# Optimization experiments

Measured on AMD Instinct MI355X. Metric: run time of the kernel, lower is better.

The kernel has to match this reference:

```python
import jax, jax.numpy as jnp
import numpy as np

GROUPS = 8
EPS = 1e-5
STRIDE_W = 2


def group_norm(x, gamma, beta, groups=GROUPS):
    B, C, H, W = x.shape
    xr = x.reshape(B, groups, C // groups, H, W)
    m = xr.mean(axis=(2, 3, 4), keepdims=True)
    v = xr.var(axis=(2, 3, 4), keepdims=True)
    xn = ((xr - m) * jax.lax.rsqrt(v + EPS)).reshape(B, C, H, W)
    return xn * gamma[None, :, None, None] + beta[None, :, None, None]


def setup_inputs() -> dict:
    key = jax.random.key(0)
    ks = jax.random.split(key, 8)
    B, Cin, Cout = 2, 128, 256
    Hin, Win = 181, 360
    Hout, Wout = 91, 180
    K, NNZ = 7, 16  # piecewise-linear (3,3) basis -> 7 basis fns; 16 nonzeros per output row
    x = jax.random.normal(ks[0], (B, Cin, Hin, Win), jnp.float32)
    psi_vals = jax.random.normal(ks[1], (K, Hout, NNZ), jnp.float32) * 0.1
    psi_hi = jax.random.randint(ks[2], (Hout, NNZ), 0, Hin)
    psi_wi = jax.random.randint(ks[3], (Hout, NNZ), 0, Win)
    weight = jax.random.normal(ks[4], (Cout, Cin, K), jnp.float32) * (1.0 / np.sqrt(Cin * K))
    bias = jnp.zeros((Cout,), jnp.float32)
    gn1_gamma = jnp.ones((Cin,), jnp.float32)
    gn1_beta = jnp.zeros((Cin,), jnp.float32)
    w1 = jax.random.normal(ks[5], (2 * Cin, Cin), jnp.float32) * (1.0 / np.sqrt(Cin))
    b1 = jnp.zeros((2 * Cin,), jnp.float32)
    w2 = jax.random.normal(ks[6], (Cin, 2 * Cin), jnp.float32) * (1.0 / np.sqrt(2 * Cin))
    b2 = jnp.zeros((Cin,), jnp.float32)
    gamma2 = jnp.ones((Cout,), jnp.float32)
    beta2 = jnp.zeros((Cout,), jnp.float32)
    return dict(x=x, psi_vals=psi_vals, psi_hi=psi_hi, psi_wi=psi_wi, weight=weight,
                bias=bias, gn1_gamma=gn1_gamma, gn1_beta=gn1_beta, w1=w1, b1=b1,
                w2=w2, b2=b2, gamma2=gamma2, beta2=beta2)


def reference(x, psi_vals, psi_hi, psi_wi, weight, bias, gn1_gamma, gn1_beta,
              w1, b1, w2, b2, gamma2, beta2):
    B, C, Hin, Win = x.shape
    K, Hout, NNZ = psi_vals.shape
    Wout = Win // STRIDE_W

    # --- FlowerBlock stand-in (norm -> 1x1 expand -> GELU -> 1x1 project) + residual ---
    h = group_norm(x, gn1_gamma, gn1_beta)
    h = jnp.einsum('oc,bchw->bohw', w1, h) + b1[None, :, None, None]
    h = jax.nn.gelu(h)
    h = jnp.einsum('oc,bchw->bohw', w2, h) + b2[None, :, None, None]
    x = h + x
    skip = x

    # --- DISCO S2 conv: sparse basis-weighted gather + channel contraction ---
    # psi is longitudinally translation-equivariant: nonzeros stored for lon 0,
    wo = jnp.arange(Wout)
    idx = psi_hi[:, None, :] * Win + (psi_wi[:, None, :] + STRIDE_W * wo[None, :, None]) % Win  # [Hout,Wout,NNZ]
    xg = x.reshape(B, C, Hin * Win)[:, :, idx]               # [B,C,Hout,Wout,NNZ] gather
    y = jnp.einsum('khn,bchwn->bckhw', psi_vals, xg)          # basis-weighted reduce
    out = jnp.einsum('ock,bckhw->bohw', weight, y) + bias[None, :, None, None]

    x_down = jax.nn.gelu(group_norm(out, gamma2, beta2))
    return (skip, x_down)
```

## Files before the change

### kernel.cpp

```cpp
#include <hip/hip_runtime.h>


#define HW      65160
#define HIN     181
#define WIN     360
#define HOUT    91
#define WOUT    180
#define CIN     128
#define COUT    256
#define KB      7
#define NNZ     16
#define N_GN1   1042560
#define N_GN2   524160
#define NPB     16380

typedef float  f32x4  __attribute__((ext_vector_type(4)));
typedef __bf16 bf16x8 __attribute__((ext_vector_type(8)));

__device__ __forceinline__ unsigned short f2b(float v){
    return __builtin_bit_cast(unsigned short, (__bf16)v);
}
__device__ __forceinline__ unsigned pkbf(float a, float b){
    return (unsigned)__builtin_bit_cast(unsigned short, (__bf16)a)
         | ((unsigned)__builtin_bit_cast(unsigned short, (__bf16)b) << 16);
}
__device__ __forceinline__ float blo(unsigned u){ return __uint_as_float(u << 16); }
__device__ __forceinline__ float bhi(unsigned u){ return __uint_as_float(u & 0xffff0000u); }

__device__ __forceinline__ float gelu_f(float v){
    float z = v * __builtin_fmaf(0.0356774081363f, v*v, 0.7978845608028654f);
    float e = __builtin_amdgcn_exp2f(-2.8853900817779268f * z);
    return v * __builtin_amdgcn_rcpf(1.0f + e);
}

__global__ __launch_bounds__(256) void k_prep(
    const float* __restrict__ x, float* __restrict__ part,
    const float* __restrict__ wsrc, unsigned short* __restrict__ wbf,
    const float* __restrict__ w2, unsigned short* __restrict__ w2b)
{
    const int blk_id = blockIdx.x;
    const int t = threadIdx.x;

    if (blk_id < 2048){
        const int bg = blk_id >> 7, blk = blk_id & 127;
        const float4* p4 = (const float4*)(x + (size_t)bg * N_GN1);
        float s = 0.f, ss = 0.f;
        for (int v = blk*256 + t; v < N_GN1/4; v += 128*256){
            float4 q = p4[v];
            s  += q.x + q.y + q.z + q.w;
            ss += q.x*q.x + q.y*q.y + q.z*q.z + q.w*q.w;
        }
        #pragma unroll
        for (int off = 32; off; off >>= 1){ s += __shfl_down(s, off); ss += __shfl_down(ss, off); }
        __shared__ float ls[4][2];
        if ((t & 63) == 0){ ls[t>>6][0] = s; ls[t>>6][1] = ss; }
        __syncthreads();
        if (t == 0){
            s  = ls[0][0] + ls[1][0] + ls[2][0] + ls[3][0];
            ss = ls[0][1] + ls[1][1] + ls[2][1] + ls[3][1];
            part[(bg*128 + blk)*2]     = s;
            part[(bg*128 + blk)*2 + 1] = ss;
        }
    } else if (blk_id < 2304){
        const int co = blk_id - 2048;
        for (int r = t; r < 896; r += 256){
            int k = r >> 7, c = r & 127;
            wbf[co*896 + r] = f2b(wsrc[co*896 + c*7 + k]);
        }
    } else {
        const int i = (blk_id - 2304)*256 + t;
        if (i < 32768) w2b[i] = f2b(w2[i]);
    }
}

__global__ __launch_bounds__(64) void k_fold(
    const float* __restrict__ part,
    const float* __restrict__ w1, const float* __restrict__ b1,
    const float* __restrict__ g1, const float* __restrict__ be1,
    unsigned short* __restrict__ w1f, float* __restrict__ b1f)
{
    const int id = blockIdx.x;
    const int b = id >> 8, oc = id & 255;
    const int l = threadIdx.x;

    float mArr[8], rArr[8];
    #pragma unroll
    for (int g = 0; g < 8; ++g){
        const int bg = b*8 + g;
        float s  = part[(bg*128 + l)*2]     + part[(bg*128 + 64 + l)*2];
        float ss = part[(bg*128 + l)*2 + 1] + part[(bg*128 + 64 + l)*2 + 1];
        #pragma unroll
        for (int off = 32; off; off >>= 1){ s += __shfl_down(s, off); ss += __shfl_down(ss, off); }
        s = __shfl(s, 0); ss = __shfl(ss, 0);
        float m = s / (float)N_GN1;
        float v = ss / (float)N_GN1 - m*m;
        mArr[g] = m;
        rArr[g] = 1.0f / sqrtf(v + 1e-5f);
    }

    float acc = 0.f;
    #pragma unroll
    for (int j = 0; j < 2; ++j){
        const int c = l + j*64;
        const int g = c >> 4;
        float a  = rArr[g] * g1[c];
        float bb = be1[c] - mArr[g]*a;
        float wv = w1[oc*128 + c];
        w1f[((size_t)b*256 + oc)*128 + c] = f2b(wv * a);
        acc += wv * bb;
    }
    #pragma unroll
    for (int off = 32; off; off >>= 1) acc += __shfl_down(acc, off);
    if (l == 0) b1f[b*256 + oc] = b1[oc] + acc;
}

__global__ __launch_bounds__(256, 4) void k_mlp(
    const float* __restrict__ x,
    const unsigned short* __restrict__ w1f, const float* __restrict__ b1f,
    const unsigned short* __restrict__ w2b, const float* __restrict__ b2,
    float* __restrict__ skip, unsigned short* __restrict__ sbf)
{
    __shared__ unsigned short xns[64*128];
    __shared__ unsigned short h1h[64*128];

    const int t = threadIdx.x;
    const int b = blockIdx.y;
    const int pix0 = blockIdx.x * 64;
    const int valid = min(64, HW - pix0);

    const int w  = t >> 6, l = t & 63;
    const int lr = l & 15, lk = l >> 4;

    {
        const int p = l;
        const unsigned sw = ((unsigned)(p & 7)) << 4;
        const float* xb = x + (size_t)b*128*HW + pix0 + p;
        #pragma unroll
        for (int i = 0; i < 8; ++i){
            const int c0 = w*32 + i*4;
            uint2 pk;
            if (p < valid){
                pk.x = pkbf(xb[(size_t)(c0+0)*HW], xb[(size_t)(c0+1)*HW]);
                pk.y = pkbf(xb[(size_t)(c0+2)*HW], xb[(size_t)(c0+3)*HW]);
            } else { pk.x = 0u; pk.y = 0u; }
            *(uint2*)((char*)xns + p*256 + (((unsigned)(c0*2)) ^ sw)) = pk;
        }
    }
    __syncthreads();

    f32x4 acc2[4][2];
    {
        const float bv0 = b2[w*32 + lr];
        const float bv1 = b2[w*32 + 16 + lr];
        #pragma unroll
        for (int pm = 0; pm < 4; ++pm){
            acc2[pm][0] = (f32x4)bv0;
            acc2[pm][1] = (f32x4)bv1;
        }
    }

    const unsigned short* w1p = w1f + (size_t)b*256*128;

    #pragma unroll
    for (int half = 0; half < 2; ++half){
        {
            f32x4 acc1[2][4];
            #pragma unroll
            for (int m = 0; m < 2; ++m){
                float4 bv = *(const float4*)(b1f + b*256 + half*128 + w*32 + m*16 + lk*4);
                #pragma unroll
                for (int nf = 0; nf < 4; ++nf) acc1[m][nf] = __builtin_bit_cast(f32x4, bv);
            }
            const unsigned short* wr = w1p + (size_t)(half*128 + w*32 + lr)*128 + lk*8;
            #pragma unroll
            for (int ks = 0; ks < 4; ++ks){
                bf16x8 af[2];
                #pragma unroll
                for (int m = 0; m < 2; ++m)
                    af[m] = __builtin_bit_cast(bf16x8, *(const uint4*)(wr + m*16*128 + ks*32));
                bf16x8 bfv[4];
                #pragma unroll
                for (int nf = 0; nf < 4; ++nf){
                    const int p = nf*16 + lr;
                    unsigned off = (unsigned)(p*256)
                                 + (((unsigned)(ks*64 + lk*16)) ^ (((unsigned)(p & 7)) << 4));
                    bfv[nf] = __builtin_bit_cast(bf16x8, *(const uint4*)((const char*)xns + off));
                }
                #pragma unroll
                for (int m = 0; m < 2; ++m)
                    #pragma unroll
                    for (int nf = 0; nf < 4; ++nf)
                        acc1[m][nf] = __builtin_amdgcn_mfma_f32_16x16x32_bf16(af[m], bfv[nf], acc1[m][nf], 0, 0, 0);
            }
            #pragma unroll
            for (int m = 0; m < 2; ++m){
                const int oc0 = w*32 + m*16 + lk*4;
                #pragma unroll
                for (int nf = 0; nf < 4; ++nf){
                    const int p = nf*16 + lr;
                    uint2 pk;
                    pk.x = pkbf(gelu_f(acc1[m][nf][0]), gelu_f(acc1[m][nf][1]));
                    pk.y = pkbf(gelu_f(acc1[m][nf][2]), gelu_f(acc1[m][nf][3]));
                    unsigned off = (unsigned)(p*256)
                                 + (((unsigned)(oc0*2)) ^ (((unsigned)(p & 7)) << 4));
                    *(uint2*)((char*)h1h + off) = pk;
                }
            }
        }
        __syncthreads();

        {
            const unsigned short* wr = w2b + (size_t)(w*32 + lr)*256 + half*128 + lk*8;
            #pragma unroll
            for (int ks = 0; ks < 4; ++ks){
                bf16x8 bfw[2];
                #pragma unroll
                for (int cn = 0; cn < 2; ++cn)
                    bfw[cn] = __builtin_bit_cast(bf16x8, *(const uint4*)(wr + cn*16*256 + ks*32));
                bf16x8 afh[4];
                #pragma unroll
                for (int pm = 0; pm < 4; ++pm){
                    const int p = pm*16 + lr;
                    unsigned off = (unsigned)(p*256)
                                 + (((unsigned)(ks*64 + lk*16)) ^ (((unsigned)(p & 7)) << 4));
                    afh[pm] = __builtin_bit_cast(bf16x8, *(const uint4*)((const char*)h1h + off));
                }
                #pragma unroll
                for (int pm = 0; pm < 4; ++pm)
                    #pragma unroll
                    for (int cn = 0; cn < 2; ++cn)
                        acc2[pm][cn] = __builtin_amdgcn_mfma_f32_16x16x32_bf16(afh[pm], bfw[cn], acc2[pm][cn], 0, 0, 0);
            }
        }
        if (half == 0) __syncthreads();
    }

    #pragma unroll
    for (int pm = 0; pm < 4; ++pm){
        const int p0 = pm*16 + lk*4;
        if (p0 < valid){
            #pragma unroll
            for (int cn = 0; cn < 2; ++cn){
                const int c = w*32 + cn*16 + lr;
                size_t base = (size_t)(b*128 + c)*HW + pix0 + p0;
                float4 o;
                #pragma unroll
                for (int r = 0; r < 4; ++r){
                    const int p = p0 + r;
                    unsigned off = (unsigned)(p*256)
                                 + (((unsigned)(c*2)) ^ (((unsigned)(p & 7)) << 4));
                    unsigned short us = *(const unsigned short*)((const char*)xns + off);
                    ((float*)&o)[r] = acc2[pm][cn][r] + blo((unsigned)us);
                }
                *(float4*)(skip + base) = o;
                if (sbf){
                    unsigned short* sp = sbf + ((size_t)b*HW + pix0 + p0)*128 + c;
                    sp[0]   = f2b(o.x);
                    sp[128] = f2b(o.y);
                    sp[256] = f2b(o.z);
                    sp[384] = f2b(o.w);
                }
            }
        }
    }
}

__global__ __launch_bounds__(256) void k_dfuse(
    const unsigned short* __restrict__ sbf,
    const float* __restrict__ psi_v, const int* __restrict__ psi_hi, const int* __restrict__ psi_wi,
    const unsigned short* __restrict__ wbf, const float* __restrict__ bias,
    unsigned short* __restrict__ xdb, float* __restrict__ part)
{
    __shared__ unsigned short yT[64*256];
    __shared__ float psis[2][112];
    __shared__ int   his[2][16], wis[2][16];

    const int flat = blockIdx.x + 256*blockIdx.y;
    const int rem  = (flat & 7)*64 + (flat >> 3);
    const int nt   = rem & 255;
    const int b    = rem >> 8;
    const int n0   = nt*64;

    const int t = threadIdx.x;
    const int w = t >> 6, l = t & 63;
    const int lr = l & 15, lk = l >> 4;

    const int ho0 = n0 / WOUT;
    const int ho1 = min((n0 + 63) / WOUT, HOUT - 1);

    if (t < 112)        psis[0][t]       = psi_v[((t >> 4)*HOUT + ho0)*NNZ + (t & 15)];
    else if (t < 224)   psis[1][t - 112] = psi_v[(((t - 112) >> 4)*HOUT + ho1)*NNZ + ((t - 112) & 15)];
    else if (t < 240){  his[0][t - 224] = psi_hi[ho0*NNZ + t - 224];
                        wis[0][t - 224] = psi_wi[ho0*NNZ + t - 224]; }
    else             {  his[1][t - 240] = psi_hi[ho1*NNZ + t - 240];
                        wis[1][t - 240] = psi_wi[ho1*NNZ + t - 240]; }
    __syncthreads();

    const int row = t >> 2, cq = t & 3;
    const int n_c = min(n0 + row, NPB - 1);
    const int ho  = n_c / WOUT;
    const int wo  = n_c - ho*WOUT;
    const int sel = (ho == ho0) ? 0 : 1;
    const unsigned swr = ((unsigned)(row & 7)) << 4;

    int offs[16];
    #pragma unroll
    for (int n = 0; n < 16; ++n){
        int wv = wis[sel][n] + 2*wo;
        wv = (wv >= WIN) ? (wv - WIN) : wv;
        offs[n] = his[sel][n]*WIN + wv;
    }
    const unsigned short* sb = sbf + (size_t)b * HW * 128;

    f32x4 acc[4][4];
    #pragma unroll
    for (int i = 0; i < 4; ++i)
        #pragma unroll
        for (int j = 0; j < 4; ++j) acc[i][j] = (f32x4)0.f;

    #pragma unroll 1
    for (int cc = 0; cc < 4; ++cc){
        __syncthreads();
        {
            const int cl0 = cq*8;
            float ya[8][7];
            #pragma unroll
            for (int ci = 0; ci < 8; ++ci)
                #pragma unroll
                for (int k = 0; k < 7; ++k) ya[ci][k] = 0.f;

            #pragma unroll 4
            for (int n = 0; n < 16; ++n){
                uint4 q = *(const uint4*)(sb + (size_t)offs[n]*128 + cc*32 + cl0);
                float g0 = blo(q.x), g1 = bhi(q.x), g2 = blo(q.y), g3 = bhi(q.y);
                float g4 = blo(q.z), g5 = bhi(q.z), g6 = blo(q.w), g7 = bhi(q.w);
                #pragma unroll
                for (int k = 0; k < 7; ++k){
                    float pv = psis[sel][k*16 + n];
                    ya[0][k] += pv*g0; ya[1][k] += pv*g1; ya[2][k] += pv*g2; ya[3][k] += pv*g3;
                    ya[4][k] += pv*g4; ya[5][k] += pv*g5; ya[6][k] += pv*g6; ya[7][k] += pv*g7;
                }
            }
            char* rowp = (char*)yT + row*512;
            #pragma unroll
            for (int k = 0; k < 7; ++k){
                uint4 pk;
                pk.x = pkbf(ya[0][k], ya[1][k]);
                pk.y = pkbf(ya[2][k], ya[3][k]);
                pk.z = pkbf(ya[4][k], ya[5][k]);
                pk.w = pkbf(ya[6][k], ya[7][k]);
                *(uint4*)(rowp + (((unsigned)(k*64 + cl0*2)) ^ swr)) = pk;
            }
        }
        __syncthreads();

        const unsigned short* wr = wbf + (size_t)(w*64 + lr)*896 + cc*32 + lk*8;
        #pragma unroll
        for (int k = 0; k < 7; ++k){
            bf16x8 af[4];
            #pragma unroll
            for (int i = 0; i < 4; ++i){
                const int r = i*16 + lr;
                unsigned off = (unsigned)(r*512)
                             + (((unsigned)(k*64 + lk*16)) ^ (((unsigned)(r & 7)) << 4));
                af[i] = __builtin_bit_cast(bf16x8, *(const uint4*)((const char*)yT + off));
            }
            bf16x8 bfw[4];
            #pragma unroll
            for (int j = 0; j < 4; ++j)
                bfw[j] = __builtin_bit_cast(bf16x8, *(const uint4*)(wr + (size_t)j*16*896 + k*128));
            #pragma unroll
            for (int i = 0; i < 4; ++i)
                #pragma unroll
                for (int j = 0; j < 4; ++j)
                    acc[i][j] = __builtin_amdgcn_mfma_f32_16x16x32_bf16(af[i], bfw[j], acc[i][j], 0, 0, 0);
        }
    }

    float s[2] = {0.f, 0.f}, ss[2] = {0.f, 0.f};
    #pragma unroll
    for (int j = 0; j < 4; ++j){
        const int co = w*64 + j*16 + lr;
        const float bv = bias[co];
        unsigned short* outp = xdb + (size_t)(b*256 + co)*NPB;
        const int jp = j >> 1;
        #pragma unroll
        for (int i = 0; i < 4; ++i){
            const int nb = n0 + i*16 + lk*4;
            if (nb < NPB){
                float o0 = acc[i][j][0] + bv, o1 = acc[i][j][1] + bv;
                float o2 = acc[i][j][2] + bv, o3 = acc[i][j][3] + bv;
                uint2 pk; pk.x = pkbf(o0, o1); pk.y = pkbf(o2, o3);
                *(uint2*)(outp + nb) = pk;
                s[jp]  += o0 + o1 + o2 + o3;
                ss[jp] += o0*o0 + o1*o1 + o2*o2 + o3*o3;
            }
        }
    }
    #pragma unroll
    for (int off = 32; off; off >>= 1){
        s[0] += __shfl_down(s[0], off); ss[0] += __shfl_down(ss[0], off);
        s[1] += __shfl_down(s[1], off); ss[1] += __shfl_down(ss[1], off);
    }
    if (l == 0){
        const int bid = b*256 + nt;
        const int g0 = w*2;
        part[(bid*8 + g0 + 0)*2]     = s[0];
        part[(bid*8 + g0 + 0)*2 + 1] = ss[0];
        part[(bid*8 + g0 + 1)*2]     = s[1];
        part[(bid*8 + g0 + 1)*2 + 1] = ss[1];
    }
}

__global__ __launch_bounds__(256) void k_gn2_apply_s(const unsigned short* __restrict__ xdb,
                                                     float* __restrict__ outd,
                                                     const float* __restrict__ part,
                                                     const float* __restrict__ g2a,
                                                     const float* __restrict__ be2){
    __shared__ float ls[16][2];
    const int t = threadIdx.x;
    {
        const int grp = t >> 4;
        const int bb = grp >> 3, g = grp & 7;
        const int l16 = t & 15;
        float s = 0.f, ssum = 0.f;
        #pragma unroll
        for (int j = 0; j < 16; ++j){
            const int nt = l16 + j*16;
            const int idx = ((bb*256 + nt)*8 + g)*2;
            s    += part[idx];
            ssum += part[idx + 1];
        }
        #pragma unroll
        for (int off = 8; off; off >>= 1){
            s    += __shfl_xor(s, off);
            ssum += __shfl_xor(ssum, off);
        }
        if (l16 == 0){
            float m = s / (float)N_GN2;
            float v = ssum / (float)N_GN2 - m*m;
            ls[grp][0] = m;
            ls[grp][1] = 1.0f / sqrtf(v + 1e-5f);
        }
    }
    __syncthreads();

    const int gid = blockIdx.x*256 + t;
    const int stride = gridDim.x*256;
    for (int v = gid; v < 2096640; v += stride){
        uint2 q = ((const uint2*)xdb)[v];
        int i  = v << 2;
        int bc = i / 16380;
        int co = bc & 255, b = bc >> 8;
        const int grp = b*8 + (co >> 5);
        float m  = ls[grp][0];
        float r  = ls[grp][1];
        float a  = r * g2a[co];
        float bb = be2[co] - m*a;
        float4 o;
        o.x = gelu_f(__builtin_fmaf(blo(q.x), a, bb));
        o.y = gelu_f(__builtin_fmaf(bhi(q.x), a, bb));
        o.z = gelu_f(__builtin_fmaf(blo(q.y), a, bb));
        o.w = gelu_f(__builtin_fmaf(bhi(q.y), a, bb));
        ((float4*)outd)[v] = o;
    }
}

__global__ __launch_bounds__(256, 2) void k_disco_fb(
    const float* __restrict__ skip,
    const float* __restrict__ psi_v, const int* __restrict__ psi_hi, const int* __restrict__ psi_wi,
    const unsigned short* __restrict__ wbf, const float* __restrict__ bias,
    float* __restrict__ xdown, float* __restrict__ part)
{
    __shared__ unsigned short yT[96*256];

    const int t   = threadIdx.x;
    const int woh = blockIdx.x;
    const int ho  = blockIdx.y;
    const int z   = blockIdx.z;
    const int b   = z >> 1, coh = z & 1;
    const int co0 = coh * 128;
    const int wo0 = woh * 90;

    const int w  = t >> 6;
    const int l  = t & 63;
    const int wm = w >> 1, wn = w & 1;

    const int wol = t & 31;
    const int cq  = t >> 5;
    const unsigned sw = (unsigned)(wol & 7) << 4;

    const float* skipb = skip + (size_t)b * (128*HW);

    f32x4 acc[4][3];
    #pragma unroll
    for (int m = 0; m < 4; ++m)
        #pragma unroll
        for (int nf = 0; nf < 3; ++nf) acc[m][nf] = (f32x4)0.f;

    #pragma unroll 1
    for (int cc = 0; cc < 4; ++cc){
        __syncthreads();
        const float* bp0 = skipb + (size_t)(cc*32 + cq*4 + 0)*HW;
        const float* bp1 = skipb + (size_t)(cc*32 + cq*4 + 1)*HW;
        const float* bp2 = skipb + (size_t)(cc*32 + cq*4 + 2)*HW;
        const float* bp3 = skipb + (size_t)(cc*32 + cq*4 + 3)*HW;

        float ya[3][4][7];
        #pragma unroll
        for (int wj = 0; wj < 3; ++wj)
            #pragma unroll
            for (int ci = 0; ci < 4; ++ci)
                #pragma unroll
                for (int k = 0; k < 7; ++k) ya[wj][ci][k] = 0.f;

        #pragma unroll 2
        for (int n = 0; n < NNZ; ++n){
            const int hi = psi_hi[ho*NNZ + n];
            const int wi = psi_wi[ho*NNZ + n];
            float ps[7];
            #pragma unroll
            for (int k = 0; k < 7; ++k) ps[k] = psi_v[(k*HOUT + ho)*NNZ + n];
            const int rowb = hi * WIN;
            #pragma unroll
            for (int wj = 0; wj < 3; ++wj){
                int wv = wi + 2*(wo0 + wol + 32*wj);
                wv = (wv >= 720) ? (wv - 720) : (wv >= 360 ? (wv - 360) : wv);
                const int off = rowb + wv;
                float g0 = bp0[off], g1 = bp1[off], g2 = bp2[off], g3 = bp3[off];
                #pragma unroll
                for (int k = 0; k < 7; ++k){
                    float pv = ps[k];
                    ya[wj][0][k] += pv*g0; ya[wj][1][k] += pv*g1;
                    ya[wj][2][k] += pv*g2; ya[wj][3][k] += pv*g3;
                }
            }
        }
        #pragma unroll
        for (int wj = 0; wj < 3; ++wj){
            char* rowp = (char*)yT + (wol + 32*wj)*512;
            #pragma unroll
            for (int k = 0; k < 7; ++k){
                unsigned base = ((unsigned)(k*64 + cq*8)) ^ sw;
                *(unsigned*)(rowp + base)     = pkbf(ya[wj][0][k], ya[wj][1][k]);
                *(unsigned*)(rowp + base + 4) = pkbf(ya[wj][2][k], ya[wj][3][k]);
            }
        }
        __syncthreads();

        const unsigned short* wrow = wbf + (size_t)(co0 + wm*64 + (l & 15))*896
                                         + cc*32 + ((l >> 4) << 3);
        #pragma unroll
        for (int k = 0; k < 7; ++k){
            bf16x8 af[4];
            #pragma unroll
            for (int m = 0; m < 4; ++m)
                af[m] = __builtin_bit_cast(bf16x8,
                          *(const uint4*)(wrow + (size_t)m*16*896 + k*128));
            bf16x8 bfv[3];
            #pragma unroll
            for (int nf = 0; nf < 3; ++nf){
                const int wo_l = wn*48 + nf*16 + (l & 15);
                unsigned off = (unsigned)(wo_l*512)
                             + (((unsigned)(k*64) + ((unsigned)(l >> 4) << 4))
                                ^ ((unsigned)(wo_l & 7) << 4));
                bfv[nf] = __builtin_bit_cast(bf16x8, *(const uint4*)((const char*)yT + off));
            }
            #pragma unroll
            for (int m = 0; m < 4; ++m)
                #pragma unroll
                for (int nf = 0; nf < 3; ++nf)
                    acc[m][nf] = __builtin_amdgcn_mfma_f32_16x16x32_bf16(af[m], bfv[nf], acc[m][nf], 0, 0, 0);
        }
    }

    float s[2] = {0.f, 0.f}, ss[2] = {0.f, 0.f};
    #pragma unroll
    for (int m = 0; m < 4; ++m){
        const int pair = m >> 1;
        const int cob = co0 + wm*64 + m*16 + ((l >> 4) << 2);
        float4 bv = *(const float4*)(bias + cob);
        #pragma unroll
        for (int nf = 0; nf < 3; ++nf){
            const int wo_t = wn*48 + nf*16 + (l & 15);
            if (wo_t < 90){
                #pragma unroll
                for (int r = 0; r < 4; ++r){
                    float v = acc[m][nf][r] + ((const float*)&bv)[r];
                    xdown[((size_t)(b*256 + cob + r)*HOUT + ho)*WOUT + wo0 + wo_t] = v;
                    s[pair] += v; ss[pair] += v*v;
                }
            }
        }
    }
    #pragma unroll
    for (int off = 32; off; off >>= 1){
        s[0] += __shfl_down(s[0], off); ss[0] += __shfl_down(ss[0], off);
        s[1] += __shfl_down(s[1], off); ss[1] += __shfl_down(ss[1], off);
    }
    if (l == 0){
        const int tid = (z*91 + ho)*2 + woh;
        part[(tid*8 + w*2 + 0)*2]     = s[0];
        part[(tid*8 + w*2 + 0)*2 + 1] = ss[0];
        part[(tid*8 + w*2 + 1)*2]     = s[1];
        part[(tid*8 + w*2 + 1)*2 + 1] = ss[1];
    }
}

__global__ __launch_bounds__(256) void k_gn2_final_fb(const float* __restrict__ part,
                                                      float* __restrict__ stat){
    const int bg = blockIdx.x, b = bg >> 3, g = bg & 7, t = threadIdx.x;
    const int coh = g >> 2, gl = g & 3, wm = gl >> 1, pair = gl & 1;
    float s = 0.f, ss = 0.f;
    for (int i = t; i < 364; i += 256){
        int ho = i >> 2, r = i & 3, woh = r >> 1, wn = r & 1;
        int tid = (((b*2 + coh)*91 + ho)*2 + woh);
        int slot = (wm*2 + wn)*2 + pair;
        s  += part[(tid*8 + slot)*2];
        ss += part[(tid*8 + slot)*2 + 1];
    }
    #pragma unroll
    for (int off = 32; off; off >>= 1){ s += __shfl_down(s, off); ss += __shfl_down(ss, off); }
    __shared__ float ls[4][2];
    if ((t & 63) == 0){ ls[t>>6][0] = s; ls[t>>6][1] = ss; }
    __syncthreads();
    if (t == 0){
        s  = ls[0][0] + ls[1][0] + ls[2][0] + ls[3][0];
        ss = ls[0][1] + ls[1][1] + ls[2][1] + ls[3][1];
        float m = s / (float)N_GN2;
        float v = ss / (float)N_GN2 - m*m;
        stat[bg*2]     = m;
        stat[bg*2 + 1] = 1.0f / sqrtf(v + 1e-5f);
    }
}

__global__ __launch_bounds__(256) void k_gn2_apply(float* __restrict__ xd,
                                                   const float* __restrict__ stat,
                                                   const float* __restrict__ g2a,
                                                   const float* __restrict__ be2){
    const int gid = blockIdx.x*256 + threadIdx.x;
    const int stride = gridDim.x*256;
    for (int v = gid; v < 2096640; v += stride){
        float4 q = ((float4*)xd)[v];
        int i  = v << 2;
        int bc = i / 16380;
        int co = bc & 255, b = bc >> 8;
        float m  = stat[(b*8 + (co >> 5))*2];
        float r  = stat[(b*8 + (co >> 5))*2 + 1];
        float a  = r * g2a[co];
        float bb = be2[co] - m*a;
        q.x = gelu_f(__builtin_fmaf(q.x, a, bb));
        q.y = gelu_f(__builtin_fmaf(q.y, a, bb));
        q.z = gelu_f(__builtin_fmaf(q.z, a, bb));
        q.w = gelu_f(__builtin_fmaf(q.w, a, bb));
        ((float4*)xd)[v] = q;
    }
}

extern "C" void kernel_launch(void* const* d_in, const int* in_sizes, int n_in,
                              void* d_out, int out_size, void* d_ws, size_t ws_size,
                              hipStream_t stream){
    const float* x      = (const float*)d_in[0];
    const float* psi_v  = (const float*)d_in[1];
    const int*   psi_hi = (const int*)d_in[2];
    const int*   psi_wi = (const int*)d_in[3];
    const float* weight = (const float*)d_in[4];
    const float* bias   = (const float*)d_in[5];
    const float* g1     = (const float*)d_in[6];
    const float* be1    = (const float*)d_in[7];
    const float* w1     = (const float*)d_in[8];
    const float* b1     = (const float*)d_in[9];
    const float* w2     = (const float*)d_in[10];
    const float* b2     = (const float*)d_in[11];
    const float* g2     = (const float*)d_in[12];
    const float* be2    = (const float*)d_in[13];

    float* skip  = (float*)d_out;
    float* xdown = skip + 16680960;

    float* ws       = (float*)d_ws;
    float* gn1_part = ws;
    float* gn2_part = ws + 4128;
    float* gn2_stat = ws + 15776;
    unsigned short* wbf = (unsigned short*)(ws + 15808);
    unsigned short* w1f = (unsigned short*)(ws + 130496);
    float*          b1f = ws + 163264;
    unsigned short* w2b = (unsigned short*)(ws + 163776);
    unsigned short* sbf = (unsigned short*)(ws + 180160);
    unsigned short* xdb = sbf;
    const size_t need = 8520640ull * 4ull;

    const bool split = (ws_size >= need);

    k_prep       <<<2432, 256, 0, stream>>>(x, gn1_part, weight, wbf, w2, w2b);
    k_fold       <<<512, 64, 0, stream>>>(gn1_part, w1, b1, g1, be1, w1f, b1f);
    k_mlp        <<<dim3(1019, 2), 256, 0, stream>>>(x, w1f, b1f, w2b, b2,
                                                     skip, split ? sbf : (unsigned short*)nullptr);
    if (split){
        k_dfuse     <<<dim3(256, 2), 256, 0, stream>>>(sbf, psi_v, psi_hi, psi_wi,
                                                       wbf, bias, xdb, gn2_part);
        k_gn2_apply_s<<<512, 256, 0, stream>>>(xdb, xdown, gn2_part, g2, be2);
    } else {
        k_disco_fb <<<dim3(2, 91, 4), 256, 0, stream>>>(skip, psi_v, psi_hi, psi_wi,
                                                        wbf, bias, xdown, gn2_part);
        k_gn2_final_fb<<<16, 256, 0, stream>>>(gn2_part, gn2_stat);
        k_gn2_apply<<<2048, 256, 0, stream>>>(xdown, gn2_stat, g2, be2);
    }
}
```

Before: 148.8 us.

## Double k_dfuse block to 512 threads and give xdb its own buffer

Raises the DISCO fused kernel from 256 to 512 threads per block. Each thread now gathers 4 channels instead of 8, and each wave computes 32 output channels instead of 64. This halves per-thread register accumulators and gather work, and the GN2 partial sums move to one group per wave. The bf16 output buffer is also moved out of the region that aliases the gathered skip buffer, which removes a read/write overlap between blocks but raises the workspace requirement. If the workspace is too small, the slower fallback path will be taken.

```diff
diff --git a/kernel.cpp b/kernel.cpp
--- a/kernel.cpp
+++ b/kernel.cpp
@@ -265,7 +265,7 @@
     }
 }
 
-__global__ __launch_bounds__(256) void k_dfuse(
+__global__ __launch_bounds__(512) void k_dfuse(
     const unsigned short* __restrict__ sbf,
     const float* __restrict__ psi_v, const int* __restrict__ psi_hi, const int* __restrict__ psi_wi,
     const unsigned short* __restrict__ wbf, const float* __restrict__ bias,
@@ -292,11 +292,11 @@
     else if (t < 224)   psis[1][t - 112] = psi_v[(((t - 112) >> 4)*HOUT + ho1)*NNZ + ((t - 112) & 15)];
     else if (t < 240){  his[0][t - 224] = psi_hi[ho0*NNZ + t - 224];
                         wis[0][t - 224] = psi_wi[ho0*NNZ + t - 224]; }
-    else             {  his[1][t - 240] = psi_hi[ho1*NNZ + t - 240];
+    else if (t < 256){  his[1][t - 240] = psi_hi[ho1*NNZ + t - 240];
                         wis[1][t - 240] = psi_wi[ho1*NNZ + t - 240]; }
     __syncthreads();
 
-    const int row = t >> 2, cq = t & 3;
+    const int row = t >> 3, cq = t & 7;
     const int n_c = min(n0 + row, NPB - 1);
     const int ho  = n_c / WOUT;
     const int wo  = n_c - ho*WOUT;
@@ -312,49 +312,46 @@
     }
     const unsigned short* sb = sbf + (size_t)b * HW * 128;
 
-    f32x4 acc[4][4];
+    f32x4 acc[4][2];
     #pragma unroll
     for (int i = 0; i < 4; ++i)
         #pragma unroll
-        for (int j = 0; j < 4; ++j) acc[i][j] = (f32x4)0.f;
+        for (int j = 0; j < 2; ++j) acc[i][j] = (f32x4)0.f;
 
     #pragma unroll 1
     for (int cc = 0; cc < 4; ++cc){
         __syncthreads();
         {
-            const int cl0 = cq*8;
-            float ya[8][7];
-            #pragma unroll
-            for (int ci = 0; ci < 8; ++ci)
+            const int cl0 = cq*4;
+            float ya[4][7];
+            #pragma unroll
+            for (int ci = 0; ci < 4; ++ci)
                 #pragma unroll
                 for (int k = 0; k < 7; ++k) ya[ci][k] = 0.f;
 
             #pragma unroll 4
             for (int n = 0; n < 16; ++n){
-                uint4 q = *(const uint4*)(sb + (size_t)offs[n]*128 + cc*32 + cl0);
+                uint2 q = *(const uint2*)(sb + (size_t)offs[n]*128 + cc*32 + cl0);
                 float g0 = blo(q.x), g1 = bhi(q.x), g2 = blo(q.y), g3 = bhi(q.y);
-                float g4 = blo(q.z), g5 = bhi(q.z), g6 = blo(q.w), g7 = bhi(q.w);
                 #pragma unroll
                 for (int k = 0; k < 7; ++k){
                     float pv = psis[sel][k*16 + n];
-                    ya[0][k] += pv*g0; ya[1][k] += pv*g1; ya[2][k] += pv*g2; ya[3][k] += pv*g3;
-                    ya[4][k] += pv*g4; ya[5][k] += pv*g5; ya[6][k] += pv*g6; ya[7][k] += pv*g7;
+                    ya[0][k] += pv*g0; ya[1][k] += pv*g1;
+                    ya[2][k] += pv*g2; ya[3][k] += pv*g3;
                 }
             }
             char* rowp = (char*)yT + row*512;
             #pragma unroll
             for (int k = 0; k < 7; ++k){
-                uint4 pk;
+                uint2 pk;
                 pk.x = pkbf(ya[0][k], ya[1][k]);
                 pk.y = pkbf(ya[2][k], ya[3][k]);
-                pk.z = pkbf(ya[4][k], ya[5][k]);
-                pk.w = pkbf(ya[6][k], ya[7][k]);
-                *(uint4*)(rowp + (((unsigned)(k*64 + cl0*2)) ^ swr)) = pk;
+                *(uint2*)(rowp + (((unsigned)(k*64 + cl0*2)) ^ swr)) = pk;
             }
         }
         __syncthreads();
 
-        const unsigned short* wr = wbf + (size_t)(w*64 + lr)*896 + cc*32 + lk*8;
+        const unsigned short* wr = wbf + (size_t)(w*32 + lr)*896 + cc*32 + lk*8;
         #pragma unroll
         for (int k = 0; k < 7; ++k){
             bf16x8 af[4];
@@ -365,25 +362,24 @@
                              + (((unsigned)(k*64 + lk*16)) ^ (((unsigned)(r & 7)) << 4));
                 af[i] = __builtin_bit_cast(bf16x8, *(const uint4*)((const char*)yT + off));
             }
-            bf16x8 bfw[4];
-            #pragma unroll
-            for (int j = 0; j < 4; ++j)
+            bf16x8 bfw[2];
+            #pragma unroll
+            for (int j = 0; j < 2; ++j)
                 bfw[j] = __builtin_bit_cast(bf16x8, *(const uint4*)(wr + (size_t)j*16*896 + k*128));
             #pragma unroll
             for (int i = 0; i < 4; ++i)
                 #pragma unroll
-                for (int j = 0; j < 4; ++j)
+                for (int j = 0; j < 2; ++j)
                     acc[i][j] = __builtin_amdgcn_mfma_f32_16x16x32_bf16(af[i], bfw[j], acc[i][j], 0, 0, 0);
         }
     }
 
-    float s[2] = {0.f, 0.f}, ss[2] = {0.f, 0.f};
-    #pragma unroll
-    for (int j = 0; j < 4; ++j){
-        const int co = w*64 + j*16 + lr;
+    float s = 0.f, ss = 0.f;
+    #pragma unroll
+    for (int j = 0; j < 2; ++j){
+        const int co = w*32 + j*16 + lr;
         const float bv = bias[co];
         unsigned short* outp = xdb + (size_t)(b*256 + co)*NPB;
-        const int jp = j >> 1;
         #pragma unroll
         for (int i = 0; i < 4; ++i){
             const int nb = n0 + i*16 + lk*4;
@@ -392,23 +388,19 @@
                 float o2 = acc[i][j][2] + bv, o3 = acc[i][j][3] + bv;
                 uint2 pk; pk.x = pkbf(o0, o1); pk.y = pkbf(o2, o3);
                 *(uint2*)(outp + nb) = pk;
-                s[jp]  += o0 + o1 + o2 + o3;
-                ss[jp] += o0*o0 + o1*o1 + o2*o2 + o3*o3;
+                s  += o0 + o1 + o2 + o3;
+                ss += o0*o0 + o1*o1 + o2*o2 + o3*o3;
             }
         }
     }
     #pragma unroll
     for (int off = 32; off; off >>= 1){
-        s[0] += __shfl_down(s[0], off); ss[0] += __shfl_down(ss[0], off);
-        s[1] += __shfl_down(s[1], off); ss[1] += __shfl_down(ss[1], off);
+        s += __shfl_down(s, off); ss += __shfl_down(ss, off);
     }
     if (l == 0){
         const int bid = b*256 + nt;
-        const int g0 = w*2;
-        part[(bid*8 + g0 + 0)*2]     = s[0];
-        part[(bid*8 + g0 + 0)*2 + 1] = ss[0];
-        part[(bid*8 + g0 + 1)*2]     = s[1];
-        part[(bid*8 + g0 + 1)*2 + 1] = ss[1];
+        part[(bid*8 + w)*2]     = s;
+        part[(bid*8 + w)*2 + 1] = ss;
     }
 }
 
@@ -687,8 +679,8 @@
     float*          b1f = ws + 163264;
     unsigned short* w2b = (unsigned short*)(ws + 163776);
     unsigned short* sbf = (unsigned short*)(ws + 180160);
-    unsigned short* xdb = sbf;
-    const size_t need = 8520640ull * 4ull;
+    unsigned short* xdb = (unsigned short*)(ws + 8520640);
+    const size_t need = 12713920ull * 4ull;
 
     const bool split = (ws_size >= need);
 
@@ -697,7 +689,7 @@
     k_mlp        <<<dim3(1019, 2), 256, 0, stream>>>(x, w1f, b1f, w2b, b2,
                                                      skip, split ? sbf : (unsigned short*)nullptr);
     if (split){
-        k_dfuse     <<<dim3(256, 2), 256, 0, stream>>>(sbf, psi_v, psi_hi, psi_wi,
+        k_dfuse     <<<dim3(256, 2), 512, 0, stream>>>(sbf, psi_v, psi_hi, psi_wi,
                                                        wbf, bias, xdb, gn2_part);
         k_gn2_apply_s<<<512, 256, 0, stream>>>(xdb, xdown, gn2_part, g2, be2);
     } else {
```

Result: no change. 151.6 us (median of 2 runs) (+1.9%).
